# Kernel optimization log

Measured on AMD Instinct MI355X. Metric: run time of the kernel, lower is better.

The kernel has to match this reference:

```python
import jax, jax.numpy as jnp
import numpy as np

N_NODES = 50000


def gcn_conv(x, W, b, src, dst, n_nodes):
    """PyG GCNConv: add self-loops, symmetric norm, linear, scatter-add, bias."""
    h = x @ W  # [N, out]
    # degree with self-loops: deg[i] = 1 + (# edges with dst == i)
    deg = 1.0 + jax.ops.segment_sum(jnp.ones_like(dst, dtype=h.dtype), dst,
                                    num_segments=n_nodes)
    dinv = jax.lax.rsqrt(deg)  # deg^{-1/2}
    # per-edge norm for non-self-loop edges
    norm = dinv[src] * dinv[dst]  # [E]
    agg = jax.ops.segment_sum(h[src] * norm[:, None], dst,
                              num_segments=n_nodes)
    # self-loop contribution: dinv[i]*dinv[i]*h[i] = h[i]/deg[i]
    agg = agg + h * (dinv * dinv)[:, None]
    return agg + b


def setup_inputs() -> dict:
    key = jax.random.key(0)
    ks = jax.random.split(key, 6)
    x = jax.random.normal(ks[0], (N_NODES, 512), dtype=jnp.float32)
    edge_index = jax.random.randint(ks[1], (2, 800000), 0, N_NODES,
                                    dtype=jnp.int64)
    W1 = jax.random.normal(ks[2], (512, 256), dtype=jnp.float32) * (512 ** -0.5)
    b1 = jnp.zeros((256,), dtype=jnp.float32)
    W2 = jax.random.normal(ks[3], (256, 256), dtype=jnp.float32) * (256 ** -0.5)
    b2 = jnp.zeros((256,), dtype=jnp.float32)
    W3 = jax.random.normal(ks[4], (256, 64), dtype=jnp.float32) * (256 ** -0.5)
    b3 = jnp.zeros((64,), dtype=jnp.float32)
    return {"x": x, "edge_index": edge_index, "W1": W1, "b1": b1,
            "W2": W2, "b2": b2, "W3": W3, "b3": b3}


def reference(x, edge_index, W1, b1, W2, b2, W3, b3):
    src, dst = edge_index[0], edge_index[1]
    n = x.shape[0]
    h = gcn_conv(x, W1, b1, src, dst, n)
    h = jax.nn.relu(h)  # dropout is a no-op in eval mode
    h = gcn_conv(h, W2, b2, src, dst, n)
    h = jax.nn.relu(h)
    h = gcn_conv(h, W3, b3, src, dst, n)
    # faithful to the original: softmax then log_softmax
    h = jax.nn.softmax(h, axis=1)
    return jax.nn.log_softmax(h, axis=1)
```

## Files before the change

kernel.cpp:

```cpp
#include <hip/hip_runtime.h>
#include <cstdint>
#include <cstddef>

typedef float  f32x4  __attribute__((ext_vector_type(4)));
typedef float  f32x2  __attribute__((ext_vector_type(2)));

__device__ __forceinline__ unsigned int f2fp8x4(float a, float b, float c, float d) {
  int v = __builtin_amdgcn_cvt_pk_fp8_f32(a, b, 0, false);
  v = __builtin_amdgcn_cvt_pk_fp8_f32(c, d, v, true);
  return (unsigned int)v;
}
__device__ __forceinline__ unsigned char f2fp8(float f) {
  return (unsigned char)(__builtin_amdgcn_cvt_pk_fp8_f32(f, f, 0, false) & 0xff);
}
__device__ __forceinline__ void fp8x8_to_f32(uint2 d, float* f) {
  f32x2 a = __builtin_amdgcn_cvt_pk_f32_fp8((int)d.x, false);
  f32x2 b = __builtin_amdgcn_cvt_pk_f32_fp8((int)d.x, true);
  f32x2 c = __builtin_amdgcn_cvt_pk_f32_fp8((int)d.y, false);
  f32x2 e = __builtin_amdgcn_cvt_pk_f32_fp8((int)d.y, true);
  f[0] = a.x; f[1] = a.y; f[2] = b.x; f[3] = b.y;
  f[4] = c.x; f[5] = c.y; f[6] = e.x; f[7] = e.y;
}
__device__ __forceinline__ void fp8x4_to_f32(unsigned int d, float* f) {
  f32x2 a = __builtin_amdgcn_cvt_pk_f32_fp8((int)d, false);
  f32x2 b = __builtin_amdgcn_cvt_pk_f32_fp8((int)d, true);
  f[0] = a.x; f[1] = a.y; f[2] = b.x; f[3] = b.y;
}
__device__ __forceinline__ void fp8x16_to_f32(uint4 d, float* f) {
  uint2 lo; lo.x = d.x; lo.y = d.y;
  uint2 hi; hi.x = d.z; hi.y = d.w;
  fp8x8_to_f32(lo, f);
  fp8x8_to_f32(hi, f + 8);
}

__device__ __forceinline__ void async_copy16(const void* g, void* l) {
  __builtin_amdgcn_global_load_lds(
      (const __attribute__((address_space(1))) unsigned int*)g,
      (__attribute__((address_space(3))) unsigned int*)l, 16, 0, 0);
}

#define NN 50000
#define MPAD 50048
#define SCAN_BLOCKS 196

#define XB_BLOCKS 6256
#define WB_BLOCKS 52

__global__ __launch_bounds__(256) void gcn_prep_k(
    const float* __restrict__ X, unsigned char* __restrict__ x8,
    const float* __restrict__ W1, const float* __restrict__ W2,
    const float* __restrict__ W3,
    unsigned char* __restrict__ W1T8, unsigned char* __restrict__ W2T8,
    unsigned char* __restrict__ W3T8, int* __restrict__ cnt) {
  int b = blockIdx.x;
  if (b < SCAN_BLOCKS) {
    int ii = b * 256 + threadIdx.x;
    if (ii < NN) cnt[ii] = 0;
  }
  if (b < XB_BLOCKS) {
    int idx16 = (b * 256 + threadIdx.x) * 16;
    int row = idx16 >> 9;
    uint4 o;
    if (row < NN) {
      const float* s = &X[idx16];
      float4 v0 = *(const float4*)s;
      float4 v1 = *(const float4*)(s + 4);
      float4 v2 = *(const float4*)(s + 8);
      float4 v3 = *(const float4*)(s + 12);
      o.x = f2fp8x4(v0.x, v0.y, v0.z, v0.w);
      o.y = f2fp8x4(v1.x, v1.y, v1.z, v1.w);
      o.z = f2fp8x4(v2.x, v2.y, v2.z, v2.w);
      o.w = f2fp8x4(v3.x, v3.y, v3.z, v3.w);
    } else {
      o = uint4{0, 0, 0, 0};
    }
    *(uint4*)&x8[idx16] = o;
  } else {
    int wb = b - XB_BLOCKS;
    if (wb < 32) {
      int idx16 = (wb * 256 + threadIdx.x) * 16;
      int n = idx16 >> 9;
      float f[16];
#pragma unroll
      for (int j = 0; j < 16; j++) f[j] = W1[(size_t)((idx16 & 511) + j) * 256 + n];
      uint4 o;
      o.x = f2fp8x4(f[0], f[1], f[2], f[3]);
      o.y = f2fp8x4(f[4], f[5], f[6], f[7]);
      o.z = f2fp8x4(f[8], f[9], f[10], f[11]);
      o.w = f2fp8x4(f[12], f[13], f[14], f[15]);
      *(uint4*)&W1T8[idx16] = o;
    } else if (wb < 48) {
      int idx16 = ((wb - 32) * 256 + threadIdx.x) * 16;
      int n = idx16 >> 8;
      float f[16];
#pragma unroll
      for (int j = 0; j < 16; j++) f[j] = W2[(size_t)((idx16 & 255) + j) * 256 + n];
      uint4 o;
      o.x = f2fp8x4(f[0], f[1], f[2], f[3]);
      o.y = f2fp8x4(f[4], f[5], f[6], f[7]);
      o.z = f2fp8x4(f[8], f[9], f[10], f[11]);
      o.w = f2fp8x4(f[12], f[13], f[14], f[15]);
      *(uint4*)&W2T8[idx16] = o;
    } else {
      int idx16 = ((wb - 48) * 256 + threadIdx.x) * 16;
      int n = idx16 >> 8;
      float f[16];
#pragma unroll
      for (int j = 0; j < 16; j++) f[j] = W3[(size_t)((idx16 & 255) + j) * 64 + n];
      uint4 o;
      o.x = f2fp8x4(f[0], f[1], f[2], f[3]);
      o.y = f2fp8x4(f[4], f[5], f[6], f[7]);
      o.z = f2fp8x4(f[8], f[9], f[10], f[11]);
      o.w = f2fp8x4(f[12], f[13], f[14], f[15]);
      *(uint4*)&W3T8[idx16] = o;
    }
  }
}

__global__ void gcn_count_k(const int* __restrict__ dst, int* __restrict__ cnt, int E) {
  int e = blockIdx.x * 256 + threadIdx.x;
  if (e < E) atomicAdd(&cnt[dst[e]], 1);
}

__global__ __launch_bounds__(256) void gcn_scan_blocks_k(
    const int* __restrict__ cnt, int* __restrict__ blockSum, int nNodes) {
  __shared__ int sw[4];
  int t = threadIdx.x;
  int i = blockIdx.x * 256 + t;
  int v = (i < nNodes) ? cnt[i] : 0;
  for (int off = 32; off > 0; off >>= 1) v += __shfl_down(v, off);
  if ((t & 63) == 0) sw[t >> 6] = v;
  __syncthreads();
  if (t == 0) blockSum[blockIdx.x] = sw[0] + sw[1] + sw[2] + sw[3];
}

__global__ __launch_bounds__(256) void gcn_scan_tops_k(
    int* __restrict__ blockSum, int nBlocks) {
  __shared__ int sb[256];
  int t = threadIdx.x;
  int v = (t < nBlocks) ? blockSum[t] : 0;
  sb[t] = v;
  __syncthreads();
  for (int off = 1; off < 256; off <<= 1) {
    int x = (t >= off) ? sb[t - off] : 0;
    __syncthreads();
    sb[t] += x;
    __syncthreads();
  }
  if (t < nBlocks) blockSum[t] = sb[t] - v;
}

__global__ __launch_bounds__(256) void gcn_scan_final_k(
    const int* __restrict__ cnt, const int* __restrict__ blockSum,
    int* __restrict__ rs, int* __restrict__ cur, float* __restrict__ dinv,
    int nNodes, int E) {
  __shared__ int sb[256];
  int t = threadIdx.x;
  int i = blockIdx.x * 256 + t;
  int v = (i < nNodes) ? cnt[i] : 0;
  sb[t] = v;
  __syncthreads();
  for (int off = 1; off < 256; off <<= 1) {
    int x = (t >= off) ? sb[t - off] : 0;
    __syncthreads();
    sb[t] += x;
    __syncthreads();
  }
  if (i < nNodes) {
    int off = blockSum[blockIdx.x] + sb[t] - v;
    rs[i] = off; cur[i] = off;
    dinv[i] = rsqrtf(1.0f + (float)v);
  }
  if (i == 0) rs[nNodes] = E;
}

__global__ void gcn_scatter_k(const int* __restrict__ src, const int* __restrict__ dst,
                              int* __restrict__ cur, const float* __restrict__ dinv,
                              int2* __restrict__ e2, int E) {
  int e = blockIdx.x * 256 + threadIdx.x;
  if (e < E) {
    int d = dst[e];
    int s = src[e];
    int p = atomicAdd(&cur[d], 1);
    int2 v; v.x = s; v.y = __float_as_int(dinv[s] * dinv[d]);
    e2[p] = v;
  }
}

template<int BN, int WTN>
__global__ __launch_bounds__(256) void gcn_gemm_f8_db_k(
    const unsigned char* __restrict__ A8,
    const unsigned char* __restrict__ Bt8,
    unsigned char* __restrict__ C8,
    int K, int N) {
  static_assert(BN == 128, "db kernel assumes uniform 2 global_load_lds per thread");
  __shared__ __align__(16) unsigned char lds_a[2][128 * 32];
  __shared__ __align__(16) unsigned char lds_b[2][BN * 32];
  const int t = threadIdx.x;
  const int wave = t >> 6, lane = t & 63;
  const int wr = wave >> 1, wc = wave & 1;
  const int quad = lane >> 4, lrow = lane & 15;
  const int m0 = blockIdx.x * 128;
  const int n0 = blockIdx.y * BN;

  f32x4 acc[4][WTN] = {};

  auto stage = [&](int buf, int k0) {
    int r = t >> 1, c = (t & 1) * 16;
    async_copy16(&A8[(size_t)(m0 + r) * K + k0 + c], &lds_a[buf][t * 16]);
    async_copy16(&Bt8[(size_t)(n0 + r) * K + k0 + c], &lds_b[buf][t * 16]);
  };
  auto compute = [&](int buf) {
    long af[4], bfr[WTN];
#pragma unroll
    for (int mt = 0; mt < 4; mt++)
      af[mt] = *(const long*)&lds_a[buf][(wr * 64 + mt * 16 + lrow) * 32 + quad * 8];
#pragma unroll
    for (int nt = 0; nt < WTN; nt++)
      bfr[nt] = *(const long*)&lds_b[buf][(wc * (BN / 2) + nt * 16 + lrow) * 32 + quad * 8];
#pragma unroll
    for (int mt = 0; mt < 4; mt++)
#pragma unroll
      for (int nt = 0; nt < WTN; nt++)
        acc[mt][nt] = __builtin_amdgcn_mfma_f32_16x16x32_fp8_fp8(af[mt], bfr[nt], acc[mt][nt], 0, 0, 0);
  };

  stage(0, 0);
  int curb = 0;
  int k0 = 0;
  for (; k0 + 32 < K; k0 += 32) {
    stage(curb ^ 1, k0 + 32);
    asm volatile("s_waitcnt vmcnt(2)" ::: "memory");
    __builtin_amdgcn_s_barrier();
    asm volatile("" ::: "memory");
    compute(curb);
    asm volatile("" ::: "memory");
    __builtin_amdgcn_s_barrier();
    curb ^= 1;
  }
  asm volatile("s_waitcnt vmcnt(0)" ::: "memory");
  __builtin_amdgcn_s_barrier();
  asm volatile("" ::: "memory");
  compute(curb);

#pragma unroll
  for (int mt = 0; mt < 4; mt++)
#pragma unroll
    for (int nt = 0; nt < WTN; nt++)
#pragma unroll
      for (int r = 0; r < 4; r++) {
        int row = m0 + wr * 64 + mt * 16 + quad * 4 + r;
        int col = n0 + wc * (BN / 2) + nt * 16 + lrow;
        C8[(size_t)row * N + col] = f2fp8(acc[mt][nt][r]);
      }
}

template<int BN, int WTN>
__global__ __launch_bounds__(256) void gcn_gemm_f8_s_k(
    const unsigned char* __restrict__ A8, const unsigned char* __restrict__ Bt8,
    unsigned char* __restrict__ C8, int K, int N) {
  __shared__ __align__(16) unsigned char lds_a[128 * 32];
  __shared__ __align__(16) unsigned char lds_b[BN * 32];
  const int t = threadIdx.x;
  const int wave = t >> 6, lane = t & 63;
  const int wr = wave >> 1, wc = wave & 1;
  const int quad = lane >> 4, lrow = lane & 15;
  const int m0 = blockIdx.x * 128;
  const int n0 = blockIdx.y * BN;

  f32x4 acc[4][WTN] = {};

  for (int k0 = 0; k0 < K; k0 += 32) {
    __syncthreads();
    {
      int r = t >> 1, c = (t & 1) * 16;
      async_copy16(&A8[(size_t)(m0 + r) * K + k0 + c], &lds_a[t * 16]);
    }
    for (int q = t; q < BN * 2; q += 256) {
      int r = q >> 1, c = (q & 1) * 16;
      async_copy16(&Bt8[(size_t)(n0 + r) * K + k0 + c], &lds_b[q * 16]);
    }
    __syncthreads();
    long af[4], bfr[WTN];
#pragma unroll
    for (int mt = 0; mt < 4; mt++)
      af[mt] = *(const long*)&lds_a[(wr * 64 + mt * 16 + lrow) * 32 + quad * 8];
#pragma unroll
    for (int nt = 0; nt < WTN; nt++)
      bfr[nt] = *(const long*)&lds_b[(wc * (BN / 2) + nt * 16 + lrow) * 32 + quad * 8];
#pragma unroll
    for (int mt = 0; mt < 4; mt++)
#pragma unroll
      for (int nt = 0; nt < WTN; nt++)
        acc[mt][nt] = __builtin_amdgcn_mfma_f32_16x16x32_fp8_fp8(af[mt], bfr[nt], acc[mt][nt], 0, 0, 0);
  }

#pragma unroll
  for (int mt = 0; mt < 4; mt++)
#pragma unroll
    for (int nt = 0; nt < WTN; nt++)
#pragma unroll
      for (int r = 0; r < 4; r++) {
        int row = m0 + wr * 64 + mt * 16 + quad * 4 + r;
        int col = n0 + wc * (BN / 2) + nt * 16 + lrow;
        C8[(size_t)row * N + col] = f2fp8(acc[mt][nt][r]);
      }
}

template<int D>
__global__ __launch_bounds__(256) void gcn_agg_relu_k(
    const unsigned char* __restrict__ h8, const int* __restrict__ rs,
    const int2* __restrict__ e2, const float* __restrict__ dinv,
    const float* __restrict__ bias, unsigned char* __restrict__ out8, int nNodes) {
  int wave = threadIdx.x >> 6, lane = threadIdx.x & 63;
  int i = blockIdx.x * 4 + wave;
  if (i >= nNodes) return;
  int q = lane >> 4, sub = lane & 15;
  int f0 = sub * 16;
  float di = dinv[i];
  uint4 dself = *(const uint4*)&h8[(size_t)i * D + f0];
  float sv[16];
  fp8x16_to_f32(dself, sv);
  float wself = (q == 0) ? di * di : 0.0f;
  float acc[16];
#pragma unroll
  for (int j = 0; j < 16; j++) acc[j] = sv[j] * wself;

  int e0 = rs[i], e1 = rs[i + 1];
  int nIter = (e1 - e0 + 15) >> 4;
  int e = e0 + q;
  for (int k = 0; k < nIter; k++) {
    int idx[4]; float w[4];
#pragma unroll
    for (int u = 0; u < 4; u++) {
      int ee = e + 4 * u;
      bool v = ee < e1;
      int2 pr = e2[v ? ee : e0];
      idx[u] = v ? pr.x : i;
      w[u] = v ? __int_as_float(pr.y) : 0.0f;
    }
    uint4 d0 = *(const uint4*)&h8[(size_t)idx[0] * D + f0];
    uint4 d1 = *(const uint4*)&h8[(size_t)idx[1] * D + f0];
    uint4 d2 = *(const uint4*)&h8[(size_t)idx[2] * D + f0];
    uint4 d3 = *(const uint4*)&h8[(size_t)idx[3] * D + f0];
    float r[16];
    fp8x16_to_f32(d0, r);
#pragma unroll
    for (int j = 0; j < 16; j++) acc[j] += r[j] * w[0];
    fp8x16_to_f32(d1, r);
#pragma unroll
    for (int j = 0; j < 16; j++) acc[j] += r[j] * w[1];
    fp8x16_to_f32(d2, r);
#pragma unroll
    for (int j = 0; j < 16; j++) acc[j] += r[j] * w[2];
    fp8x16_to_f32(d3, r);
#pragma unroll
    for (int j = 0; j < 16; j++) acc[j] += r[j] * w[3];
    e += 16;
  }
#pragma unroll
  for (int j = 0; j < 16; j++) {
    acc[j] += __shfl_xor(acc[j], 16);
    acc[j] += __shfl_xor(acc[j], 32);
  }
  if (q == 0) {
    float4 bb0 = *(const float4*)&bias[f0];
    float4 bb1 = *(const float4*)&bias[f0 + 4];
    float4 bb2 = *(const float4*)&bias[f0 + 8];
    float4 bb3 = *(const float4*)&bias[f0 + 12];
    float bv[16] = {bb0.x, bb0.y, bb0.z, bb0.w, bb1.x, bb1.y, bb1.z, bb1.w,
                    bb2.x, bb2.y, bb2.z, bb2.w, bb3.x, bb3.y, bb3.z, bb3.w};
    float r[16];
#pragma unroll
    for (int j = 0; j < 16; j++) {
      float z = acc[j] + bv[j];
      r[j] = z > 0.0f ? z : 0.0f;
    }
    uint4 o;
    o.x = f2fp8x4(r[0], r[1], r[2], r[3]);
    o.y = f2fp8x4(r[4], r[5], r[6], r[7]);
    o.z = f2fp8x4(r[8], r[9], r[10], r[11]);
    o.w = f2fp8x4(r[12], r[13], r[14], r[15]);
    *(uint4*)&out8[(size_t)i * D + f0] = o;
  }
}

__global__ __launch_bounds__(256) void gcn_agg_final_k(
    const unsigned char* __restrict__ h8, const int* __restrict__ rs,
    const int2* __restrict__ e2, const float* __restrict__ dinv,
    const float* __restrict__ bias, float* __restrict__ out, int nNodes) {
  int wave = threadIdx.x >> 6, lane = threadIdx.x & 63;
  int i = blockIdx.x * 4 + wave;
  if (i >= nNodes) return;
  int qtr = lane >> 4, sub = lane & 15;
  int f0 = sub * 4;
  float di = dinv[i];
  unsigned int dself = *(const unsigned int*)&h8[(size_t)i * 64 + f0];
  float sv[4];
  fp8x4_to_f32(dself, sv);
  float wself = (qtr == 0) ? di * di : 0.0f;
  float acc[4];
#pragma unroll
  for (int j = 0; j < 4; j++) acc[j] = sv[j] * wself;

  int e0 = rs[i], e1 = rs[i + 1];
  int nIter = (e1 - e0 + 7) >> 3;
  int e = e0 + qtr;
  for (int k = 0; k < nIter; k++) {
    int idx[2]; float w[2];
#pragma unroll
    for (int u = 0; u < 2; u++) {
      int ee = e + 4 * u;
      bool v = ee < e1;
      int2 pr = e2[v ? ee : e0];
      idx[u] = v ? pr.x : i;
      w[u] = v ? __int_as_float(pr.y) : 0.0f;
    }
    unsigned int d0 = *(const unsigned int*)&h8[(size_t)idx[0] * 64 + f0];
    unsigned int d1 = *(const unsigned int*)&h8[(size_t)idx[1] * 64 + f0];
    float r0[4], r1[4];
    fp8x4_to_f32(d0, r0); fp8x4_to_f32(d1, r1);
#pragma unroll
    for (int j = 0; j < 4; j++)
      acc[j] += r0[j] * w[0] + r1[j] * w[1];
    e += 8;
  }
#pragma unroll
  for (int j = 0; j < 4; j++) {
    acc[j] += __shfl_xor(acc[j], 16);
    acc[j] += __shfl_xor(acc[j], 32);
    acc[j] += bias[f0 + j];
  }
  float m = fmaxf(fmaxf(acc[0], acc[1]), fmaxf(acc[2], acc[3]));
#pragma unroll
  for (int off = 8; off > 0; off >>= 1) m = fmaxf(m, __shfl_xor(m, off));
  float ex[4], s = 0.0f;
#pragma unroll
  for (int j = 0; j < 4; j++) { ex[j] = __expf(acc[j] - m); s += ex[j]; }
#pragma unroll
  for (int off = 8; off > 0; off >>= 1) s += __shfl_xor(s, off);
  float rcs = 1.0f / s;
  float p[4], s2 = 0.0f;
#pragma unroll
  for (int j = 0; j < 4; j++) { p[j] = ex[j] * rcs; s2 += __expf(p[j]); }
#pragma unroll
  for (int off = 8; off > 0; off >>= 1) s2 += __shfl_xor(s2, off);
  float ls = __logf(s2);
  if (qtr == 0) {
    float4 o; o.x = p[0] - ls; o.y = p[1] - ls; o.z = p[2] - ls; o.w = p[3] - ls;
    *(float4*)&out[(size_t)i * 64 + f0] = o;
  }
}

extern "C" void kernel_launch(void* const* d_in, const int* in_sizes, int n_in,
                              void* d_out, int out_size, void* d_ws, size_t ws_size,
                              hipStream_t stream) {
  const float* x    = (const float*)d_in[0];
  const int*   eidx = (const int*)d_in[1];
  const float* W1   = (const float*)d_in[2];
  const float* b1   = (const float*)d_in[3];
  const float* W2   = (const float*)d_in[4];
  const float* b2   = (const float*)d_in[5];
  const float* W3   = (const float*)d_in[6];
  const float* b3   = (const float*)d_in[7];
  float* out = (float*)d_out;

  const int E = in_sizes[1] / 2;
  const int* src = eidx;
  const int* dst = eidx + E;

  char* p = (char*)d_ws;
  auto alloc = [&](size_t bytes) -> void* {
    void* r = (void*)p;
    p += (bytes + 255) & ~(size_t)255;
    return r;
  };
  unsigned char*  x8   = (unsigned char*)alloc((size_t)MPAD * 512);
  unsigned char*  g8   = (unsigned char*)alloc((size_t)MPAD * 256);
  unsigned char*  a8   = (unsigned char*)alloc((size_t)MPAD * 256);
  unsigned char*  g83  = (unsigned char*)alloc((size_t)MPAD * 64);
  unsigned char*  W1T8 = (unsigned char*)alloc((size_t)256 * 512);
  unsigned char*  W2T8 = (unsigned char*)alloc((size_t)256 * 256);
  unsigned char*  W3T8 = (unsigned char*)alloc((size_t)64 * 256);
  int*   cnt  = (int*)alloc((size_t)NN * 4);
  int*   rs   = (int*)alloc((size_t)(NN + 1) * 4);
  int*   cur  = (int*)alloc((size_t)NN * 4);
  float* dinv = (float*)alloc((size_t)NN * 4);
  int2*  e2   = (int2*)alloc((size_t)E * 8);
  int*   bsum = (int*)alloc((size_t)SCAN_BLOCKS * 4);

  const int EB = (E + 255) / 256;
  gcn_prep_k<<<XB_BLOCKS + WB_BLOCKS, 256, 0, stream>>>(
      x, x8, W1, W2, W3, W1T8, W2T8, W3T8, cnt);
  gcn_count_k<<<EB, 256, 0, stream>>>(dst, cnt, E);
  gcn_scan_blocks_k<<<SCAN_BLOCKS, 256, 0, stream>>>(cnt, bsum, NN);
  gcn_scan_tops_k<<<1, 256, 0, stream>>>(bsum, SCAN_BLOCKS);
  gcn_scan_final_k<<<SCAN_BLOCKS, 256, 0, stream>>>(cnt, bsum, rs, cur, dinv, NN, E);
  gcn_scatter_k<<<EB, 256, 0, stream>>>(src, dst, cur, dinv, e2, E);

  const int MB = MPAD / 128;
  gcn_gemm_f8_db_k<128, 4><<<dim3(MB, 2), 256, 0, stream>>>(x8, W1T8, g8, 512, 256);
  gcn_agg_relu_k<256><<<(NN + 3) / 4, 256, 0, stream>>>(g8, rs, e2, dinv, b1, a8, NN);
  gcn_gemm_f8_db_k<128, 4><<<dim3(MB, 2), 256, 0, stream>>>(a8, W2T8, g8, 256, 256);
  gcn_agg_relu_k<256><<<(NN + 3) / 4, 256, 0, stream>>>(g8, rs, e2, dinv, b2, a8, NN);
  gcn_gemm_f8_s_k<64, 2><<<dim3(MB, 1), 256, 0, stream>>>(a8, W3T8, g83, 256, 64);
  gcn_agg_final_k<<<(NN + 3) / 4, 256, 0, stream>>>(g83, rs, e2, dinv, b3, out, NN);

  (void)n_in; (void)out_size; (void)ws_size;
}
```

Measured before the change: 412.8 us.

## Fold symmetric norm into GEMM epilogue and build CSR via atomic ranks

Factors the per-edge weight dinv[s]*dinv[d] out of aggregation: each GEMM now scales its output rows by dinv, and the aggregation applies dinv[i] once at the end. The edge list therefore stores only 4-byte source indices instead of index/weight pairs, which halves edge-list traffic in the three aggregation passes. The count kernel is folded into prep, where each atomic also records the edge's rank, so the scatter needs no second atomic pass. Scaling before the fp8 quantisation changes rounding slightly, and the prep kernel now also carries the edge-count atomics.

After: 388.3 us. 1.06x faster.

```diff
diff --git a/kernel.cpp b/kernel.cpp
--- a/kernel.cpp
+++ b/kernel.cpp
@@ -46,16 +46,22 @@
 #define XB_BLOCKS 6256
 #define WB_BLOCKS 52
 
+__global__ __launch_bounds__(256) void gcn_zero_k(int* __restrict__ cnt) {
+  int i = blockIdx.x * 256 + threadIdx.x;
+  if (i < NN) cnt[i] = 0;
+}
+
 __global__ __launch_bounds__(256) void gcn_prep_k(
     const float* __restrict__ X, unsigned char* __restrict__ x8,
     const float* __restrict__ W1, const float* __restrict__ W2,
     const float* __restrict__ W3,
     unsigned char* __restrict__ W1T8, unsigned char* __restrict__ W2T8,
-    unsigned char* __restrict__ W3T8, int* __restrict__ cnt) {
+    unsigned char* __restrict__ W3T8,
+    const int* __restrict__ dst, int* __restrict__ cnt, int* __restrict__ rank, int E) {
   int b = blockIdx.x;
-  if (b < SCAN_BLOCKS) {
-    int ii = b * 256 + threadIdx.x;
-    if (ii < NN) cnt[ii] = 0;
+  {
+    int e = b * 256 + threadIdx.x;
+    if (e < E) rank[e] = atomicAdd(&cnt[dst[e]], 1);
   }
   if (b < XB_BLOCKS) {
     int idx16 = (b * 256 + threadIdx.x) * 16;
@@ -117,11 +123,6 @@
   }
 }
 
-__global__ void gcn_count_k(const int* __restrict__ dst, int* __restrict__ cnt, int E) {
-  int e = blockIdx.x * 256 + threadIdx.x;
-  if (e < E) atomicAdd(&cnt[dst[e]], 1);
-}
-
 __global__ __launch_bounds__(256) void gcn_scan_blocks_k(
     const int* __restrict__ cnt, int* __restrict__ blockSum, int nNodes) {
   __shared__ int sw[4];
@@ -152,8 +153,7 @@
 
 __global__ __launch_bounds__(256) void gcn_scan_final_k(
     const int* __restrict__ cnt, const int* __restrict__ blockSum,
-    int* __restrict__ rs, int* __restrict__ cur, float* __restrict__ dinv,
-    int nNodes, int E) {
+    int* __restrict__ rs, float* __restrict__ dinv, int nNodes, int E) {
   __shared__ int sb[256];
   int t = threadIdx.x;
   int i = blockIdx.x * 256 + t;
@@ -167,23 +167,21 @@
     __syncthreads();
   }
   if (i < nNodes) {
-    int off = blockSum[blockIdx.x] + sb[t] - v;
-    rs[i] = off; cur[i] = off;
+    rs[i] = blockSum[blockIdx.x] + sb[t] - v;
     dinv[i] = rsqrtf(1.0f + (float)v);
+  } else if (i < MPAD) {
+    dinv[i] = 0.0f;
   }
   if (i == 0) rs[nNodes] = E;
 }
 
 __global__ void gcn_scatter_k(const int* __restrict__ src, const int* __restrict__ dst,
-                              int* __restrict__ cur, const float* __restrict__ dinv,
-                              int2* __restrict__ e2, int E) {
+                              const int* __restrict__ rank, const int* __restrict__ rs,
+                              int* __restrict__ e4, int E) {
   int e = blockIdx.x * 256 + threadIdx.x;
   if (e < E) {
     int d = dst[e];
-    int s = src[e];
-    int p = atomicAdd(&cur[d], 1);
-    int2 v; v.x = s; v.y = __float_as_int(dinv[s] * dinv[d]);
-    e2[p] = v;
+    e4[rs[d] + rank[e]] = src[e];
   }
 }
 
@@ -191,6 +189,7 @@
 __global__ __launch_bounds__(256) void gcn_gemm_f8_db_k(
     const unsigned char* __restrict__ A8,
     const unsigned char* __restrict__ Bt8,
+    const float* __restrict__ dinv,
     unsigned char* __restrict__ C8,
     int K, int N) {
   static_assert(BN == 128, "db kernel assumes uniform 2 global_load_lds per thread");
@@ -246,19 +245,21 @@
 #pragma unroll
   for (int mt = 0; mt < 4; mt++)
 #pragma unroll
-    for (int nt = 0; nt < WTN; nt++)
-#pragma unroll
-      for (int r = 0; r < 4; r++) {
-        int row = m0 + wr * 64 + mt * 16 + quad * 4 + r;
+    for (int r = 0; r < 4; r++) {
+      int row = m0 + wr * 64 + mt * 16 + quad * 4 + r;
+      float dv = dinv[row];
+#pragma unroll
+      for (int nt = 0; nt < WTN; nt++) {
         int col = n0 + wc * (BN / 2) + nt * 16 + lrow;
-        C8[(size_t)row * N + col] = f2fp8(acc[mt][nt][r]);
+        C8[(size_t)row * N + col] = f2fp8(acc[mt][nt][r] * dv);
       }
+    }
 }
 
 template<int BN, int WTN>
 __global__ __launch_bounds__(256) void gcn_gemm_f8_s_k(
     const unsigned char* __restrict__ A8, const unsigned char* __restrict__ Bt8,
-    unsigned char* __restrict__ C8, int K, int N) {
+    const float* __restrict__ dinv, unsigned char* __restrict__ C8, int K, int N) {
   __shared__ __align__(16) unsigned char lds_a[128 * 32];
   __shared__ __align__(16) unsigned char lds_b[BN * 32];
   const int t = threadIdx.x;
@@ -298,19 +299,21 @@
 #pragma unroll
   for (int mt = 0; mt < 4; mt++)
 #pragma unroll
-    for (int nt = 0; nt < WTN; nt++)
-#pragma unroll
-      for (int r = 0; r < 4; r++) {
-        int row = m0 + wr * 64 + mt * 16 + quad * 4 + r;
+    for (int r = 0; r < 4; r++) {
+      int row = m0 + wr * 64 + mt * 16 + quad * 4 + r;
+      float dv = dinv[row];
+#pragma unroll
+      for (int nt = 0; nt < WTN; nt++) {
         int col = n0 + wc * (BN / 2) + nt * 16 + lrow;
-        C8[(size_t)row * N + col] = f2fp8(acc[mt][nt][r]);
+        C8[(size_t)row * N + col] = f2fp8(acc[mt][nt][r] * dv);
       }
+    }
 }
 
 template<int D>
 __global__ __launch_bounds__(256) void gcn_agg_relu_k(
-    const unsigned char* __restrict__ h8, const int* __restrict__ rs,
-    const int2* __restrict__ e2, const float* __restrict__ dinv,
+    const unsigned char* __restrict__ g8, const int* __restrict__ rs,
+    const int* __restrict__ e4, const float* __restrict__ dinv,
     const float* __restrict__ bias, unsigned char* __restrict__ out8, int nNodes) {
   int wave = threadIdx.x >> 6, lane = threadIdx.x & 63;
   int i = blockIdx.x * 4 + wave;
@@ -318,10 +321,10 @@
   int q = lane >> 4, sub = lane & 15;
   int f0 = sub * 16;
   float di = dinv[i];
-  uint4 dself = *(const uint4*)&h8[(size_t)i * D + f0];
+  uint4 dself = *(const uint4*)&g8[(size_t)i * D + f0];
   float sv[16];
   fp8x16_to_f32(dself, sv);
-  float wself = (q == 0) ? di * di : 0.0f;
+  float wself = (q == 0) ? 1.0f : 0.0f;
   float acc[16];
 #pragma unroll
   for (int j = 0; j < 16; j++) acc[j] = sv[j] * wself;
@@ -335,14 +338,13 @@
     for (int u = 0; u < 4; u++) {
       int ee = e + 4 * u;
       bool v = ee < e1;
-      int2 pr = e2[v ? ee : e0];
-      idx[u] = v ? pr.x : i;
-      w[u] = v ? __int_as_float(pr.y) : 0.0f;
-    }
-    uint4 d0 = *(const uint4*)&h8[(size_t)idx[0] * D + f0];
-    uint4 d1 = *(const uint4*)&h8[(size_t)idx[1] * D + f0];
-    uint4 d2 = *(const uint4*)&h8[(size_t)idx[2] * D + f0];
-    uint4 d3 = *(const uint4*)&h8[(size_t)idx[3] * D + f0];
+      idx[u] = v ? e4[ee] : 0;
+      w[u] = v ? 1.0f : 0.0f;
+    }
+    uint4 d0 = *(const uint4*)&g8[(size_t)idx[0] * D + f0];
+    uint4 d1 = *(const uint4*)&g8[(size_t)idx[1] * D + f0];
+    uint4 d2 = *(const uint4*)&g8[(size_t)idx[2] * D + f0];
+    uint4 d3 = *(const uint4*)&g8[(size_t)idx[3] * D + f0];
     float r[16];
     fp8x16_to_f32(d0, r);
 #pragma unroll
@@ -373,7 +375,7 @@
     float r[16];
 #pragma unroll
     for (int j = 0; j < 16; j++) {
-      float z = acc[j] + bv[j];
+      float z = di * acc[j] + bv[j];
       r[j] = z > 0.0f ? z : 0.0f;
     }
     uint4 o;
@@ -386,8 +388,8 @@
 }
 
 __global__ __launch_bounds__(256) void gcn_agg_final_k(
-    const unsigned char* __restrict__ h8, const int* __restrict__ rs,
-    const int2* __restrict__ e2, const float* __restrict__ dinv,
+    const unsigned char* __restrict__ g8, const int* __restrict__ rs,
+    const int* __restrict__ e4, const float* __restrict__ dinv,
     const float* __restrict__ bias, float* __restrict__ out, int nNodes) {
   int wave = threadIdx.x >> 6, lane = threadIdx.x & 63;
   int i = blockIdx.x * 4 + wave;
@@ -395,10 +397,10 @@
   int qtr = lane >> 4, sub = lane & 15;
   int f0 = sub * 4;
   float di = dinv[i];
-  unsigned int dself = *(const unsigned int*)&h8[(size_t)i * 64 + f0];
+  unsigned int dself = *(const unsigned int*)&g8[(size_t)i * 64 + f0];
   float sv[4];
   fp8x4_to_f32(dself, sv);
-  float wself = (qtr == 0) ? di * di : 0.0f;
+  float wself = (qtr == 0) ? 1.0f : 0.0f;
   float acc[4];
 #pragma unroll
   for (int j = 0; j < 4; j++) acc[j] = sv[j] * wself;
@@ -412,12 +414,11 @@
     for (int u = 0; u < 2; u++) {
       int ee = e + 4 * u;
       bool v = ee < e1;
-      int2 pr = e2[v ? ee : e0];
-      idx[u] = v ? pr.x : i;
-      w[u] = v ? __int_as_float(pr.y) : 0.0f;
-    }
-    unsigned int d0 = *(const unsigned int*)&h8[(size_t)idx[0] * 64 + f0];
-    unsigned int d1 = *(const unsigned int*)&h8[(size_t)idx[1] * 64 + f0];
+      idx[u] = v ? e4[ee] : 0;
+      w[u] = v ? 1.0f : 0.0f;
+    }
+    unsigned int d0 = *(const unsigned int*)&g8[(size_t)idx[0] * 64 + f0];
+    unsigned int d1 = *(const unsigned int*)&g8[(size_t)idx[1] * 64 + f0];
     float r0[4], r1[4];
     fp8x4_to_f32(d0, r0); fp8x4_to_f32(d1, r1);
 #pragma unroll
@@ -429,7 +430,7 @@
   for (int j = 0; j < 4; j++) {
     acc[j] += __shfl_xor(acc[j], 16);
     acc[j] += __shfl_xor(acc[j], 32);
-    acc[j] += bias[f0 + j];
+    acc[j] = di * acc[j] + bias[f0 + j];
   }
   float m = fmaxf(fmaxf(acc[0], acc[1]), fmaxf(acc[2], acc[3]));
 #pragma unroll
@@ -484,27 +485,27 @@
   unsigned char*  W3T8 = (unsigned char*)alloc((size_t)64 * 256);
   int*   cnt  = (int*)alloc((size_t)NN * 4);
   int*   rs   = (int*)alloc((size_t)(NN + 1) * 4);
-  int*   cur  = (int*)alloc((size_t)NN * 4);
-  float* dinv = (float*)alloc((size_t)NN * 4);
-  int2*  e2   = (int2*)alloc((size_t)E * 8);
+  int*   rank = (int*)alloc((size_t)E * 4);
+  float* dinv = (float*)alloc((size_t)MPAD * 4);
+  int*   e4   = (int*)alloc((size_t)(E + 64) * 4);
   int*   bsum = (int*)alloc((size_t)SCAN_BLOCKS * 4);
 
   const int EB = (E + 255) / 256;
+  gcn_zero_k<<<SCAN_BLOCKS, 256, 0, stream>>>(cnt);
   gcn_prep_k<<<XB_BLOCKS + WB_BLOCKS, 256, 0, stream>>>(
-      x, x8, W1, W2, W3, W1T8, W2T8, W3T8, cnt);
-  gcn_count_k<<<EB, 256, 0, stream>>>(dst, cnt, E);
+      x, x8, W1, W2, W3, W1T8, W2T8, W3T8, dst, cnt, rank, E);
   gcn_scan_blocks_k<<<SCAN_BLOCKS, 256, 0, stream>>>(cnt, bsum, NN);
   gcn_scan_tops_k<<<1, 256, 0, stream>>>(bsum, SCAN_BLOCKS);
-  gcn_scan_final_k<<<SCAN_BLOCKS, 256, 0, stream>>>(cnt, bsum, rs, cur, dinv, NN, E);
-  gcn_scatter_k<<<EB, 256, 0, stream>>>(src, dst, cur, dinv, e2, E);
+  gcn_scan_final_k<<<SCAN_BLOCKS, 256, 0, stream>>>(cnt, bsum, rs, dinv, NN, E);
+  gcn_scatter_k<<<EB, 256, 0, stream>>>(src, dst, rank, rs, e4, E);
 
   const int MB = MPAD / 128;
-  gcn_gemm_f8_db_k<128, 4><<<dim3(MB, 2), 256, 0, stream>>>(x8, W1T8, g8, 512, 256);
-  gcn_agg_relu_k<256><<<(NN + 3) / 4, 256, 0, stream>>>(g8, rs, e2, dinv, b1, a8, NN);
-  gcn_gemm_f8_db_k<128, 4><<<dim3(MB, 2), 256, 0, stream>>>(a8, W2T8, g8, 256, 256);
-  gcn_agg_relu_k<256><<<(NN + 3) / 4, 256, 0, stream>>>(g8, rs, e2, dinv, b2, a8, NN);
-  gcn_gemm_f8_s_k<64, 2><<<dim3(MB, 1), 256, 0, stream>>>(a8, W3T8, g83, 256, 64);
-  gcn_agg_final_k<<<(NN + 3) / 4, 256, 0, stream>>>(g83, rs, e2, dinv, b3, out, NN);
+  gcn_gemm_f8_db_k<128, 4><<<dim3(MB, 2), 256, 0, stream>>>(x8, W1T8, dinv, g8, 512, 256);
+  gcn_agg_relu_k<256><<<(NN + 3) / 4, 256, 0, stream>>>(g8, rs, e4, dinv, b1, a8, NN);
+  gcn_gemm_f8_db_k<128, 4><<<dim3(MB, 2), 256, 0, stream>>>(a8, W2T8, dinv, g8, 256, 256);
+  gcn_agg_relu_k<256><<<(NN + 3) / 4, 256, 0, stream>>>(g8, rs, e4, dinv, b2, a8, NN);
+  gcn_gemm_f8_s_k<64, 2><<<dim3(MB, 1), 256, 0, stream>>>(a8, W3T8, dinv, g83, 256, 64);
+  gcn_agg_final_k<<<(NN + 3) / 4, 256, 0, stream>>>(g83, rs, e4, dinv, b3, out, NN);
 
   (void)n_in; (void)out_size; (void)ws_size;
 }
```
